# Performance work log

Hardware: AMD Instinct MI355X
Metric: run time of the kernel (lower is better)

## Reference

```python
import jax, jax.numpy as jnp
import numpy as np

N = 100000          # num nodes
E = 1600000         # num edges (before self loops)
IN_C = 128
OUT_C = 64
RATIO = 0.5
NEG_SLOPE = 0.2


def setup_inputs() -> dict:
    key = jax.random.key(0)
    k1, k2, k3, k4, k5 = jax.random.split(key, 5)
    x = jax.random.normal(k1, (N, IN_C), jnp.float32)
    # edges with no self loops (module removes then re-adds self loops)
    src = jax.random.randint(k2, (E,), 0, N, dtype=jnp.int32)
    off = jax.random.randint(k3, (E,), 1, N, dtype=jnp.int32)
    tgt = (src + off) % N
    edge_index = jnp.stack([src, tgt])  # [2, E], row0=source(j), row1=target(i)
    # glorot init
    s_w = float(np.sqrt(6.0 / (IN_C + OUT_C)))
    weight = jax.random.uniform(k4, (IN_C, OUT_C), jnp.float32, -s_w, s_w)
    s_a = float(np.sqrt(6.0 / (1 + 2 * OUT_C)))
    att = jax.random.uniform(k5, (1, 2 * OUT_C), jnp.float32, -s_a, s_a)
    batch = jnp.zeros((N,), jnp.int32)  # single graph
    return {"x": x, "weight": weight, "att": att,
            "edge_index": edge_index, "batch": batch, "bn": 0}


def reference(x, weight, att, edge_index, batch, bn):
    # add self loops (static shapes: E + N edges)
    loops = jnp.arange(N, dtype=edge_index.dtype)
    src = jnp.concatenate([edge_index[0], loops])  # edge_index_j (source)
    tgt = jnp.concatenate([edge_index[1], loops])  # edge_index_i (target)

    h = x @ weight                      # [N, OUT_C]
    x_j = h[src]                        # [E+N, OUT_C] gathered source feats
    x_i = h[tgt]

    # alpha = (cat([x_i, x_j]) * att).sum(-1)
    alpha = x_i @ att[0, :OUT_C] + x_j @ att[0, OUT_C:]   # [E+N]
    alpha = jnp.where(alpha > 0, alpha, NEG_SLOPE * alpha)  # leaky_relu

    # edge-softmax grouped by target node (every node has a self loop -> no empty segment)
    m = jax.ops.segment_max(alpha, tgt, num_segments=N)
    a = jnp.exp(alpha - m[tgt])
    denom = jax.ops.segment_sum(a, tgt, num_segments=N)
    alpha = a / (denom[tgt] + 1e-16)

    # node importance = sum of attention over outgoing edges (grouped by source)
    alpha_sum = jax.ops.segment_sum(alpha, src, num_segments=N)

    # topk node selection (ratio of all nodes; single graph)
    k = int(np.ceil(RATIO * N))
    _, topk_idx = jax.lax.top_k(alpha_sum, k)
    node_mask = jnp.zeros((N,), bool).at[topk_idx].set(True)

    # filter_dn: keep edges whose both endpoints survive; mask instead of compacting
    edge_mask = node_mask[src] & node_mask[tgt]
    alpha_m = jnp.where(edge_mask, alpha, 0.0)

    # weighted scatter-add aggregation to target nodes (aggr='add')
    out = jax.ops.segment_sum(alpha_m[:, None] * x_j, tgt, num_segments=N)  # [N, OUT_C]
    # bn flag is 0 -> BatchNorm skipped
    return out, edge_mask, node_mask
```

## Files before the change

### kernel.cpp

```cpp
#include <hip/hip_runtime.h>
#include <stdint.h>

#define IN_C 128
#define OUT_C 64
#define NEG_SLOPE 0.2f
#define RB 256
#define RBINS 512
#define STAGE 8192
#define NGH (RBINS * RB)
#define NGHS (RBINS * RBINS)
#define KC 8
#define SXW 384

typedef unsigned int u32;
typedef unsigned long long u64;

__device__ __forceinline__ u32 fenc(float f) {
  u32 u = __float_as_uint(f);
  return (u & 0x80000000u) ? ~u : (u | 0x80000000u);
}
__device__ __forceinline__ u64 key64(float v, int i) {
  return (((u64)fenc(v)) << 32) | (u64)(0xffffffffu - (u32)i);
}

__global__ __launch_bounds__(256) void k_gemm(const float* __restrict__ x,
                                              const float* __restrict__ w,
                                              const float* __restrict__ att,
                                              float* __restrict__ h,
                                              float* __restrict__ ai, float* __restrict__ aj,
                                              int N) {
  __shared__ float sw[IN_C * OUT_C];
  __shared__ float sx[KC * SXW];
  int tid = threadIdx.x;
  int rbase = blockIdx.x * 256;

  for (int i = tid; i < (IN_C * OUT_C) / 4; i += 256)
    ((float4*)sw)[i] = ((const float4*)w)[i];

  int c0 = (tid & 7) * 8;
  int rg = tid >> 3;
  int sxbase = rg * 12;
  float acc[8][8];
#pragma unroll
  for (int i = 0; i < 8; i++)
#pragma unroll
    for (int j = 0; j < 8; j++) acc[i][j] = 0.f;

  int str = tid >> 1;
  int skq = tid & 1;

  for (int kb = 0; kb < IN_C; kb += KC) {
    __syncthreads();
#pragma unroll
    for (int it = 0; it < 2; ++it) {
      int r = str + it * 128;
      int grow = rbase + r;
      float4 v = make_float4(0.f, 0.f, 0.f, 0.f);
      if (grow < N) v = *(const float4*)&x[(size_t)grow * IN_C + kb + skq * 4];
      int base = (r >> 3) * 12 + (r & 7);
      sx[(skq * 4 + 0) * SXW + base] = v.x;
      sx[(skq * 4 + 1) * SXW + base] = v.y;
      sx[(skq * 4 + 2) * SXW + base] = v.z;
      sx[(skq * 4 + 3) * SXW + base] = v.w;
    }
    __syncthreads();
#pragma unroll
    for (int kl = 0; kl < KC; ++kl) {
      int kg = kb + kl;
      float xr[8], wv[8];
      *(float4*)&xr[0] = *(const float4*)&sx[kl * SXW + sxbase];
      *(float4*)&xr[4] = *(const float4*)&sx[kl * SXW + sxbase + 4];
      *(float4*)&wv[0] = *(const float4*)&sw[kg * OUT_C + c0];
      *(float4*)&wv[4] = *(const float4*)&sw[kg * OUT_C + c0 + 4];
#pragma unroll
      for (int i = 0; i < 8; ++i)
#pragma unroll
        for (int j = 0; j < 8; ++j)
          acc[i][j] += xr[i] * wv[j];
    }
  }

  float pi[8], pj[8];
#pragma unroll
  for (int i = 0; i < 8; ++i) { pi[i] = 0.f; pj[i] = 0.f; }
#pragma unroll
  for (int j = 0; j < 8; ++j) {
    float a0 = att[c0 + j], a1 = att[OUT_C + c0 + j];
#pragma unroll
    for (int i = 0; i < 8; ++i) {
      pi[i] += acc[i][j] * a0;
      pj[i] += acc[i][j] * a1;
    }
  }
#pragma unroll
  for (int o = 1; o < 8; o <<= 1) {
#pragma unroll
    for (int i = 0; i < 8; ++i) {
      pi[i] += __shfl_xor(pi[i], o);
      pj[i] += __shfl_xor(pj[i], o);
    }
  }
#pragma unroll
  for (int i = 0; i < 8; ++i) {
    int row = rbase + rg * 8 + i;
    if (row < N) {
      *(float4*)&h[(size_t)row * OUT_C + c0]     = make_float4(acc[i][0], acc[i][1], acc[i][2], acc[i][3]);
      *(float4*)&h[(size_t)row * OUT_C + c0 + 4] = make_float4(acc[i][4], acc[i][5], acc[i][6], acc[i][7]);
      if ((tid & 7) == 0) { ai[row] = pi[i]; aj[row] = pj[i]; }
    }
  }
}

__global__ __launch_bounds__(256) void k_rhist_t(const int* __restrict__ tgt,
                                                 int E, int EN, int chunk, u32* __restrict__ gh,
                                                 u32* __restrict__ hist8, u32* __restrict__ done,
                                                 u32* __restrict__ sel, u32* __restrict__ cnt, u32 k) {
  __shared__ u32 lh[RBINS];
  int tid = threadIdx.x, b = blockIdx.x;
  if (b == 0) {
    for (int i = tid; i < 2048; i += 256) hist8[i] = 0u;
    if (tid < 8) { done[tid] = 0u; cnt[tid] = 0u; }
    if (tid == 0) { sel[0] = 0u; sel[1] = 0u; sel[2] = k; sel[3] = 0u; }
  }
  for (int d = tid; d < RBINS; d += 256) lh[d] = 0u;
  __syncthreads();
  int lo = b * chunk, hi = min(lo + chunk, EN);
  for (int e = lo + tid; e < hi; e += 256) {
    int t = (e < E) ? tgt[e] : e - E;
    atomicAdd(&lh[((u32)t) >> 8], 1u);
  }
  __syncthreads();
  for (int d = tid; d < RBINS; d += 256) gh[d * RB + b] = lh[d];
}

__global__ __launch_bounds__(256) void k_scanA(const u32* __restrict__ in, u32* __restrict__ out,
                                               u32* __restrict__ bsum, int n) {
  __shared__ u32 s[256];
  int i = blockIdx.x * 256 + threadIdx.x;
  u32 v = (i < n) ? in[i] : 0u;
  s[threadIdx.x] = v;
  __syncthreads();
  for (int o = 1; o < 256; o <<= 1) {
    u32 t = (threadIdx.x >= (unsigned)o) ? s[threadIdx.x - o] : 0u;
    __syncthreads();
    s[threadIdx.x] += t;
    __syncthreads();
  }
  if (i < n) out[i] = s[threadIdx.x] - v;
  if (threadIdx.x == 255) bsum[blockIdx.x] = s[255];
}

__global__ __launch_bounds__(1024) void k_scanB(u32* __restrict__ bsum, int nb) {
  __shared__ u32 s[1024];
  int tid = threadIdx.x;
  u32 v = (tid < nb) ? bsum[tid] : 0u;
  s[tid] = v;
  __syncthreads();
  for (int o = 1; o < 1024; o <<= 1) {
    u32 t = (tid >= o) ? s[tid - o] : 0u;
    __syncthreads();
    s[tid] += t;
    __syncthreads();
  }
  if (tid < nb) bsum[tid] = s[tid] - v;
}

__global__ __launch_bounds__(256) void k_scanC(u32* __restrict__ out, const u32* __restrict__ bsum, int n) {
  int i = blockIdx.x * 256 + threadIdx.x;
  if (i < n) out[i] += bsum[blockIdx.x];
}

__global__ __launch_bounds__(256) void k_rscatter_t(const int* __restrict__ src, const int* __restrict__ tgt,
                                                    int E, int EN, int chunk,
                                                    const u32* __restrict__ gh, u32* __restrict__ bufB) {
  __shared__ u32 cnt[RBINS];
  int tid = threadIdx.x, b = blockIdx.x;
  for (int d = tid; d < RBINS; d += 256) cnt[d] = gh[d * RB + b];
  __syncthreads();
  int lo = b * chunk, hi = min(lo + chunk, EN);
  for (int e = lo + tid; e < hi; e += 256) {
    int s, t;
    if (e < E) { s = src[e]; t = tgt[e]; } else { s = t = e - E; }
    u32 p = atomicAdd(&cnt[((u32)t) >> 8], 1u);
    bufB[p] = (((u32)t & 255u) << 24) | (u32)s;
  }
}

__global__ __launch_bounds__(256) void k_rpass2(const u32* __restrict__ in, u32* __restrict__ out,
                                                const u32* __restrict__ gh, u32* __restrict__ ghs,
                                                u32* __restrict__ offT,
                                                const float* __restrict__ ai, const float* __restrict__ aj,
                                                float* __restrict__ alpha,
                                                int N, int EN) {
  __shared__ u32 hist[256];
  __shared__ u32 sc[256];
  __shared__ u32 lhs[RBINS];
  __shared__ u32 stage[STAGE];
  int tid = threadIdx.x, d = blockIdx.x;
  u32 start = gh[d * RB];
  u32 end = (d < RBINS - 1) ? gh[(d + 1) * RB] : (u32)EN;
  int sz = (int)(end - start);
  hist[tid] = 0u;
  for (int dd = tid; dd < RBINS; dd += 256) lhs[dd] = 0u;
  __syncthreads();
  for (u32 p = start + tid; p < end; p += 256) {
    u32 it = in[p];
    atomicAdd(&hist[it >> 24], 1u);
    atomicAdd(&lhs[(it & 0xffffffu) >> 8], 1u);
  }
  __syncthreads();
  for (int dd = tid; dd < RBINS; dd += 256) ghs[dd * RBINS + d] = lhs[dd];
  u32 hv = hist[tid];
  sc[tid] = hv;
  __syncthreads();
  for (int o = 1; o < 256; o <<= 1) {
    u32 t = (tid >= o) ? sc[tid - o] : 0u;
    __syncthreads();
    sc[tid] += t;
    __syncthreads();
  }
  u32 excl = sc[tid] - hv;
  int node = (d << 8) + tid;
  if (node < N) offT[node] = start + excl;
  if (node == 0) offT[N] = (u32)EN;
  hist[tid] = excl;
  __syncthreads();
  bool staged = (sz <= STAGE);
  for (u32 p = start + tid; p < end; p += 256) {
    u32 it = in[p];
    u32 lp = atomicAdd(&hist[it >> 24], 1u);
    if (staged) stage[lp] = it;
    else out[start + lp] = it;
  }
  __syncthreads();
  if (staged)
    for (int i = tid; i < sz; i += 256) out[start + i] = stage[i];
  __syncthreads();
  if (node < N) {
    int lb = (tid > 0) ? (int)sc[tid - 1] : 0;
    int le = (int)sc[tid];
    float an = ai[node];
    float mx = -1e30f;
    for (int i = lb; i < le; ++i) {
      u32 it = staged ? stage[i] : out[start + i];
      float a = an + aj[it & 0xffffffu];
      a = a > 0.f ? a : NEG_SLOPE * a;
      mx = fmaxf(mx, a);
      if (staged) stage[i] = __float_as_uint(a);
    }
    float sm = 0.f;
    for (int i = lb; i < le; ++i) {
      float a;
      if (staged) a = __uint_as_float(stage[i]);
      else {
        u32 it = out[start + i];
        a = an + aj[it & 0xffffffu];
        a = a > 0.f ? a : NEG_SLOPE * a;
      }
      float v = expf(a - mx);
      sm += v;
      if (staged) stage[i] = __float_as_uint(v);
      else alpha[start + i] = v;
    }
    float inv = 1.f / (sm + 1e-16f);
    for (int i = lb; i < le; ++i) {
      float v = staged ? __uint_as_float(stage[i]) : alpha[start + i];
      alpha[start + i] = v * inv;
    }
  }
}

__global__ __launch_bounds__(256) void k_rscatter_s(const u32* __restrict__ csr,
                                                    const float* __restrict__ alpha,
                                                    const u32* __restrict__ gh, const u32* __restrict__ ghs,
                                                    u64* __restrict__ bufB, int EN) {
  __shared__ u32 cnt[RBINS];
  int tid = threadIdx.x, d = blockIdx.x;
  for (int dd = tid; dd < RBINS; dd += 256) cnt[dd] = ghs[dd * RBINS + d];
  __syncthreads();
  u32 start = gh[d * RB];
  u32 end = (d < RBINS - 1) ? gh[(d + 1) * RB] : (u32)EN;
  for (u32 e = start + tid; e < end; e += 256) {
    u32 s = csr[e] & 0xffffffu;
    u32 p = atomicAdd(&cnt[s >> 8], 1u);
    bufB[p] = (((u64)(s & 255u)) << 32) | __float_as_uint(alpha[e]);
  }
}

__global__ __launch_bounds__(256) void k_asum_acc(const u64* __restrict__ bufB,
                                                  const u32* __restrict__ ghs,
                                                  float* __restrict__ asum, int N, int EN) {
  __shared__ float sums[256];
  int tid = threadIdx.x, d = blockIdx.x;
  u32 start = ghs[d * RBINS];
  u32 end = (d < RBINS - 1) ? ghs[(d + 1) * RBINS] : (u32)EN;
  sums[tid] = 0.f;
  __syncthreads();
  for (u32 p = start + tid; p < end; p += 256) {
    u64 it = bufB[p];
    atomicAdd(&sums[(u32)(it >> 32)], __uint_as_float((u32)it));
  }
  __syncthreads();
  int node = d * 256 + tid;
  if (node < N) asum[node] = sums[tid];
}

__global__ __launch_bounds__(256) void k_histpick(const float* __restrict__ asum,
                                                  const u32* __restrict__ list_in, const u32* __restrict__ cnt_in,
                                                  u32* __restrict__ list_out, u32* __restrict__ cnt_out,
                                                  u32* __restrict__ hist8, u32* __restrict__ done,
                                                  u32* __restrict__ sel, int N, int pass, int nblk) {
  __shared__ u32 lh[256];
  __shared__ u32 sres;
  __shared__ u32 s[256];
  int tid = threadIdx.x;
  lh[tid] = 0u;
  __syncthreads();
  u64 prefix = ((const u64*)sel)[0];
  int shift = 56 - 8 * pass;
  int n = list_in ? (int)*cnt_in : N;
  int i = blockIdx.x * 256 + tid;
  if (i < n) {
    int idx = list_in ? (int)list_in[i] : i;
    u64 k = key64(asum[idx], idx);
    bool ok = (pass == 0) || ((k >> (shift + 8)) == prefix);
    if (ok) {
      atomicAdd(&lh[(u32)(k >> shift) & 255u], 1u);
      if (list_out) {
        u32 p = atomicAdd(cnt_out, 1u);
        list_out[p] = (u32)idx;
      }
    }
  }
  __syncthreads();
  if (lh[tid]) atomicAdd(&hist8[pass * 256 + tid], lh[tid]);
  __syncthreads();
  if (tid == 0)
    sres = __hip_atomic_fetch_add(&done[pass], 1u, __ATOMIC_ACQ_REL, __HIP_MEMORY_SCOPE_AGENT);
  __syncthreads();
  if (sres == (u32)(nblk - 1)) {
    u32 krem = sel[2];
    u32 hv = __hip_atomic_load(&hist8[pass * 256 + (255 - tid)], __ATOMIC_RELAXED,
                               __HIP_MEMORY_SCOPE_AGENT);
    s[tid] = hv;
    __syncthreads();
    for (int o = 1; o < 256; o <<= 1) {
      u32 t = (tid >= o) ? s[tid - o] : 0u;
      __syncthreads();
      s[tid] += t;
      __syncthreads();
    }
    u32 cum = s[tid], prev = (tid > 0) ? s[tid - 1] : 0u;
    if (cum >= krem && prev < krem) {
      int dsel = 255 - tid;
      ((u64*)sel)[0] = (prefix << 8) | (u64)(u32)dsel;
      sel[2] = krem - prev;
    }
  }
}

__global__ __launch_bounds__(256) void k_finish(const float* __restrict__ asum,
                                                const u32* __restrict__ list, const u32* __restrict__ cntp,
                                                u32* __restrict__ sel) {
  __shared__ u64 keys[2048];
  __shared__ u32 cc;
  int tid = threadIdx.x;
  if (tid == 0) cc = 0u;
  __syncthreads();
  int n = (int)*cntp;
  u32 fsel = (u32)((const u64*)sel)[0];
  u32 krem = sel[2];
  for (int i = tid; i < n; i += 256) {
    int idx = (int)list[i];
    u64 k = key64(asum[idx], idx);
    if ((u32)(k >> 32) == fsel) {
      u32 p = atomicAdd(&cc, 1u);
      if (p < 2048) keys[p] = k;
    }
  }
  __syncthreads();
  int C = (int)min(cc, 2048u);
  for (int i = tid; i < C; i += 256) {
    u64 k = keys[i];
    u32 rank = 0;
    for (int j = 0; j < C; ++j)
      if (keys[j] > k) rank++;
    if (rank == krem - 1) ((u64*)sel)[0] = k;
  }
}

__global__ __launch_bounds__(256) void k_node_mask(const float* __restrict__ asum,
                                                   const u32* __restrict__ sel,
                                                   u32* __restrict__ nm,
                                                   float* __restrict__ out_node, int N) {
  int i = blockIdx.x * 256 + threadIdx.x;
  if (i >= N) return;
  u64 T = ((const u64*)sel)[0];
  bool m = key64(asum[i], i) >= T;
  nm[i] = m ? 1u : 0u;
  out_node[i] = m ? 1.f : 0.f;
}

__global__ __launch_bounds__(256) void k_mask(const int* __restrict__ src, const int* __restrict__ tgt,
                                              const u32* __restrict__ nm,
                                              const u32* __restrict__ csr, const float* __restrict__ alpha,
                                              float* __restrict__ out_edge, u64* __restrict__ pair,
                                              int E, int EN) {
  int e = blockIdx.x * 256 + threadIdx.x;
  if (e >= EN) return;
  int s, t;
  if (e < E) { s = src[e]; t = tgt[e]; } else { s = t = e - E; }
  out_edge[e] = (nm[s] && nm[t]) ? 1.f : 0.f;
  u32 sp = csr[e] & 0xffffffu;
  u32 ab = nm[sp] ? __float_as_uint(alpha[e]) : 0u;
  pair[e] = (((u64)sp) << 32) | ab;
}

__global__ __launch_bounds__(256) void k_aggregate(const u32* __restrict__ off,
                                                   const u64* __restrict__ pair,
                                                   const float* __restrict__ h,
                                                   const u32* __restrict__ nm,
                                                   float* __restrict__ out, int N) {
  int node = blockIdx.x * 4 + (threadIdx.x >> 6);
  int lane = threadIdx.x & 63;
  int g = lane >> 4;
  int c = lane & 15;
  if (node >= N) return;
  float4 acc = make_float4(0.f, 0.f, 0.f, 0.f);
  if (nm[node]) {
    u32 b = off[node], e2 = off[node + 1];
    for (u32 p0 = b; p0 < e2; p0 += 16) {
      u64 pr[4];
      float av[4];
      u32 sv[4];
#pragma unroll
      for (int q = 0; q < 4; ++q) {
        u32 p = p0 + q * 4 + (u32)g;
        bool ok = p < e2;
        pr[q] = pair[ok ? p : b];
        av[q] = ok ? __uint_as_float((u32)pr[q]) : 0.f;
        sv[q] = (u32)(pr[q] >> 32);
      }
      float4 hv[4];
#pragma unroll
      for (int q = 0; q < 4; ++q)
        hv[q] = *(const float4*)&h[(size_t)sv[q] * OUT_C + c * 4];
#pragma unroll
      for (int q = 0; q < 4; ++q) {
        acc.x += av[q] * hv[q].x;
        acc.y += av[q] * hv[q].y;
        acc.z += av[q] * hv[q].z;
        acc.w += av[q] * hv[q].w;
      }
    }
#pragma unroll
    for (int o = 16; o < 64; o <<= 1) {
      acc.x += __shfl_xor(acc.x, o);
      acc.y += __shfl_xor(acc.y, o);
      acc.z += __shfl_xor(acc.z, o);
      acc.w += __shfl_xor(acc.w, o);
    }
  }
  if (g == 0)
    *(float4*)&out[(size_t)node * OUT_C + c * 4] = acc;
}

extern "C" void kernel_launch(void* const* d_in, const int* in_sizes, int n_in,
                              void* d_out, int out_size, void* d_ws, size_t ws_size,
                              hipStream_t stream) {
  const float* x   = (const float*)d_in[0];
  const float* w   = (const float*)d_in[1];
  const float* att = (const float*)d_in[2];
  const int*   ei  = (const int*)d_in[3];

  int N = in_sizes[0] / IN_C;
  int E = in_sizes[3] / 2;
  int EN = E + N;
  const int* src = ei;
  const int* tgt = ei + E;

  float* out      = (float*)d_out;
  float* out_edge = out + (size_t)N * OUT_C;
  float* out_node = out_edge + (size_t)EN;

  char* p = (char*)d_ws;
  auto alloc = [&](size_t bytes) -> char* {
    char* r = p;
    p += (bytes + 255) & ~(size_t)255;
    return r;
  };
  float* h     = (float*)alloc((size_t)N * OUT_C * 4);
  float* ai    = (float*)alloc((size_t)N * 4);
  float* aj    = (float*)alloc((size_t)N * 4);
  u32*   bufA  = (u32*)alloc((size_t)EN * 4);
  u64*   bufB  = (u64*)alloc((size_t)EN * 8);
  float* alpha = (float*)alloc((size_t)EN * 4);
  u32*   offT  = (u32*)alloc((size_t)(N + 1) * 4);
  u32*   gh    = (u32*)alloc((size_t)NGH * 4);
  u32*   ghs   = (u32*)alloc((size_t)NGHS * 4);
  u32*   bsum  = (u32*)alloc(2048 * 4);
  float* asum  = (float*)alloc((size_t)N * 4);
  u32*   nm    = (u32*)alloc((size_t)N * 4);
  u32*   hist8 = (u32*)alloc(2048 * 4);
  u32*   done  = (u32*)alloc(8 * 4);
  u32*   cnt   = (u32*)alloc(8 * 4);
  u32*   sel   = (u32*)alloc(256);
  u32*   listA = (u32*)alloc((size_t)N * 4);
  u32*   listB = (u32*)alloc((size_t)N * 4);

  u32 kSel = (u32)((N + 1) / 2);
  int chunk = (EN + RB - 1) / RB;
  int nScanT = (NGH + 255) / 256;
  int nScanS = (NGHS + 255) / 256;
  int gRow = (N + 255) / 256;
  int gN = (N + 255) / 256;
  int gE = (EN + 255) / 256;
  int gNode4 = (N + 3) / 4;

  k_gemm<<<gRow, 256, 0, stream>>>(x, w, att, h, ai, aj, N);

  k_rhist_t<<<RB, 256, 0, stream>>>(tgt, E, EN, chunk, gh, hist8, done, sel, cnt, kSel);
  k_scanA<<<nScanT, 256, 0, stream>>>(gh, gh, bsum, NGH);
  k_scanB<<<1, 1024, 0, stream>>>(bsum, nScanT);
  k_scanC<<<nScanT, 256, 0, stream>>>(gh, bsum, NGH);
  k_rscatter_t<<<RB, 256, 0, stream>>>(src, tgt, E, EN, chunk, gh, (u32*)bufB);
  k_rpass2<<<RBINS, 256, 0, stream>>>((u32*)bufB, bufA, gh, ghs, offT, ai, aj, alpha, N, EN);

  k_scanA<<<nScanS, 256, 0, stream>>>(ghs, ghs, bsum, NGHS);
  k_scanB<<<1, 1024, 0, stream>>>(bsum, nScanS);
  k_scanC<<<nScanS, 256, 0, stream>>>(ghs, bsum, NGHS);
  k_rscatter_s<<<RBINS, 256, 0, stream>>>(bufA, alpha, gh, ghs, bufB, EN);
  k_asum_acc<<<RBINS, 256, 0, stream>>>(bufB, ghs, asum, N, EN);

  k_histpick<<<gN, 256, 0, stream>>>(asum, nullptr, nullptr, nullptr, nullptr,
                                     hist8, done, sel, N, 0, gN);
  k_histpick<<<gN, 256, 0, stream>>>(asum, nullptr, nullptr, listA, &cnt[1],
                                     hist8, done, sel, N, 1, gN);
  k_histpick<<<gN, 256, 0, stream>>>(asum, listA, &cnt[1], listB, &cnt[2],
                                     hist8, done, sel, N, 2, gN);
  k_histpick<<<gN, 256, 0, stream>>>(asum, listB, &cnt[2], listA, &cnt[3],
                                     hist8, done, sel, N, 3, gN);
  k_finish<<<1, 256, 0, stream>>>(asum, listA, &cnt[3], sel);

  k_node_mask<<<gN, 256, 0, stream>>>(asum, sel, nm, out_node, N);
  k_mask<<<gE, 256, 0, stream>>>(src, tgt, nm, bufA, alpha, out_edge, bufB, E, EN);
  k_aggregate<<<gNode4, 256, 0, stream>>>(offT, bufB, h, nm, out, N);
}
```

Before: 372.9 us.

## Single-pass decoupled-lookback scan, retiled GEMM, half-wave aggregation

Replaces the three-kernel scan (block scan, block-sum scan, add-back) with a single-pass decoupled-lookback scan that uses ticket-ordered blocks and per-block state flags. This removes four launches and the extra passes over the histogram arrays. The GEMM is retiled to 128-thread blocks of 128 rows with KC=16 and coalesced row loads into shared memory, and aggregation now uses 32 lanes per node with 8 gathers in flight. The lookback spin-waits and the smaller GEMM blocks, which reload the weight matrix more often, add serialisation and extra traffic in exchange.

```diff
diff --git a/kernel.cpp b/kernel.cpp
--- a/kernel.cpp
+++ b/kernel.cpp
@@ -9,8 +9,8 @@
 #define STAGE 8192
 #define NGH (RBINS * RB)
 #define NGHS (RBINS * RBINS)
-#define KC 8
-#define SXW 384
+#define KC 16
+#define GROWS 128
 
 typedef unsigned int u32;
 typedef unsigned long long u64;
@@ -23,53 +23,53 @@
   return (((u64)fenc(v)) << 32) | (u64)(0xffffffffu - (u32)i);
 }
 
-__global__ __launch_bounds__(256) void k_gemm(const float* __restrict__ x,
+__global__ __launch_bounds__(128) void k_gemm(const float* __restrict__ x,
                                               const float* __restrict__ w,
                                               const float* __restrict__ att,
                                               float* __restrict__ h,
                                               float* __restrict__ ai, float* __restrict__ aj,
                                               int N) {
   __shared__ float sw[IN_C * OUT_C];
-  __shared__ float sx[KC * SXW];
+  __shared__ float sx[KC * GROWS];
   int tid = threadIdx.x;
-  int rbase = blockIdx.x * 256;
-
-  for (int i = tid; i < (IN_C * OUT_C) / 4; i += 256)
+  int rbase = blockIdx.x * GROWS;
+
+  for (int i = tid; i < (IN_C * OUT_C) / 4; i += 128)
     ((float4*)sw)[i] = ((const float4*)w)[i];
 
-  int c0 = (tid & 7) * 8;
-  int rg = tid >> 3;
-  int sxbase = rg * 12;
+  int cg = tid & 7, rg = tid >> 3;
+  int c0 = cg * 8, r0 = rg * 8;
   float acc[8][8];
 #pragma unroll
   for (int i = 0; i < 8; i++)
 #pragma unroll
     for (int j = 0; j < 8; j++) acc[i][j] = 0.f;
 
-  int str = tid >> 1;
-  int skq = tid & 1;
-
   for (int kb = 0; kb < IN_C; kb += KC) {
     __syncthreads();
-#pragma unroll
-    for (int it = 0; it < 2; ++it) {
-      int r = str + it * 128;
-      int grow = rbase + r;
-      float4 v = make_float4(0.f, 0.f, 0.f, 0.f);
-      if (grow < N) v = *(const float4*)&x[(size_t)grow * IN_C + kb + skq * 4];
-      int base = (r >> 3) * 12 + (r & 7);
-      sx[(skq * 4 + 0) * SXW + base] = v.x;
-      sx[(skq * 4 + 1) * SXW + base] = v.y;
-      sx[(skq * 4 + 2) * SXW + base] = v.z;
-      sx[(skq * 4 + 3) * SXW + base] = v.w;
+    {
+      int grow = rbase + tid;
+      float4 v0 = make_float4(0.f,0.f,0.f,0.f), v1 = v0, v2 = v0, v3 = v0;
+      if (grow < N) {
+        const float4* xp = (const float4*)&x[(size_t)grow * IN_C + kb];
+        v0 = xp[0]; v1 = xp[1]; v2 = xp[2]; v3 = xp[3];
+      }
+      sx[ 0*GROWS + tid] = v0.x; sx[ 1*GROWS + tid] = v0.y;
+      sx[ 2*GROWS + tid] = v0.z; sx[ 3*GROWS + tid] = v0.w;
+      sx[ 4*GROWS + tid] = v1.x; sx[ 5*GROWS + tid] = v1.y;
+      sx[ 6*GROWS + tid] = v1.z; sx[ 7*GROWS + tid] = v1.w;
+      sx[ 8*GROWS + tid] = v2.x; sx[ 9*GROWS + tid] = v2.y;
+      sx[10*GROWS + tid] = v2.z; sx[11*GROWS + tid] = v2.w;
+      sx[12*GROWS + tid] = v3.x; sx[13*GROWS + tid] = v3.y;
+      sx[14*GROWS + tid] = v3.z; sx[15*GROWS + tid] = v3.w;
     }
     __syncthreads();
 #pragma unroll
     for (int kl = 0; kl < KC; ++kl) {
       int kg = kb + kl;
       float xr[8], wv[8];
-      *(float4*)&xr[0] = *(const float4*)&sx[kl * SXW + sxbase];
-      *(float4*)&xr[4] = *(const float4*)&sx[kl * SXW + sxbase + 4];
+      *(float4*)&xr[0] = *(const float4*)&sx[kl * GROWS + r0];
+      *(float4*)&xr[4] = *(const float4*)&sx[kl * GROWS + r0 + 4];
       *(float4*)&wv[0] = *(const float4*)&sw[kg * OUT_C + c0];
       *(float4*)&wv[4] = *(const float4*)&sw[kg * OUT_C + c0 + 4];
 #pragma unroll
@@ -102,11 +102,11 @@
   }
 #pragma unroll
   for (int i = 0; i < 8; ++i) {
-    int row = rbase + rg * 8 + i;
+    int row = rbase + r0 + i;
     if (row < N) {
       *(float4*)&h[(size_t)row * OUT_C + c0]     = make_float4(acc[i][0], acc[i][1], acc[i][2], acc[i][3]);
       *(float4*)&h[(size_t)row * OUT_C + c0 + 4] = make_float4(acc[i][4], acc[i][5], acc[i][6], acc[i][7]);
-      if ((tid & 7) == 0) { ai[row] = pi[i]; aj[row] = pj[i]; }
+      if (cg == 0) { ai[row] = pi[i]; aj[row] = pj[i]; }
     }
   }
 }
@@ -114,12 +114,17 @@
 __global__ __launch_bounds__(256) void k_rhist_t(const int* __restrict__ tgt,
                                                  int E, int EN, int chunk, u32* __restrict__ gh,
                                                  u32* __restrict__ hist8, u32* __restrict__ done,
-                                                 u32* __restrict__ sel, u32* __restrict__ cnt, u32 k) {
+                                                 u32* __restrict__ sel, u32* __restrict__ cnt, u32 k,
+                                                 u64* __restrict__ stateT, u64* __restrict__ stateS,
+                                                 u32* __restrict__ tickets) {
   __shared__ u32 lh[RBINS];
   int tid = threadIdx.x, b = blockIdx.x;
   if (b == 0) {
     for (int i = tid; i < 2048; i += 256) hist8[i] = 0u;
+    for (int i = tid; i < 512;  i += 256) stateT[i] = 0ull;
+    for (int i = tid; i < 1024; i += 256) stateS[i] = 0ull;
     if (tid < 8) { done[tid] = 0u; cnt[tid] = 0u; }
+    if (tid < 2) tickets[tid] = 0u;
     if (tid == 0) { sel[0] = 0u; sel[1] = 0u; sel[2] = k; sel[3] = 0u; }
   }
   for (int d = tid; d < RBINS; d += 256) lh[d] = 0u;
@@ -133,41 +138,47 @@
   for (int d = tid; d < RBINS; d += 256) gh[d * RB + b] = lh[d];
 }
 
-__global__ __launch_bounds__(256) void k_scanA(const u32* __restrict__ in, u32* __restrict__ out,
-                                               u32* __restrict__ bsum, int n) {
+__global__ __launch_bounds__(256) void k_scan(u32* __restrict__ data, int n,
+                                              u32* __restrict__ ticket, u64* __restrict__ state) {
   __shared__ u32 s[256];
-  int i = blockIdx.x * 256 + threadIdx.x;
-  u32 v = (i < n) ? in[i] : 0u;
-  s[threadIdx.x] = v;
+  __shared__ u32 sticket;
+  __shared__ u32 sprefix;
+  int tid = threadIdx.x;
+  if (tid == 0)
+    sticket = __hip_atomic_fetch_add(ticket, 1u, __ATOMIC_RELAXED, __HIP_MEMORY_SCOPE_AGENT);
+  __syncthreads();
+  u32 b = sticket;
+  int i = (int)b * 256 + tid;
+  u32 v = (i < n) ? data[i] : 0u;
+  s[tid] = v;
   __syncthreads();
   for (int o = 1; o < 256; o <<= 1) {
-    u32 t = (threadIdx.x >= (unsigned)o) ? s[threadIdx.x - o] : 0u;
-    __syncthreads();
-    s[threadIdx.x] += t;
-    __syncthreads();
-  }
-  if (i < n) out[i] = s[threadIdx.x] - v;
-  if (threadIdx.x == 255) bsum[blockIdx.x] = s[255];
-}
-
-__global__ __launch_bounds__(1024) void k_scanB(u32* __restrict__ bsum, int nb) {
-  __shared__ u32 s[1024];
-  int tid = threadIdx.x;
-  u32 v = (tid < nb) ? bsum[tid] : 0u;
-  s[tid] = v;
-  __syncthreads();
-  for (int o = 1; o < 1024; o <<= 1) {
     u32 t = (tid >= o) ? s[tid - o] : 0u;
     __syncthreads();
     s[tid] += t;
     __syncthreads();
   }
-  if (tid < nb) bsum[tid] = s[tid] - v;
-}
-
-__global__ __launch_bounds__(256) void k_scanC(u32* __restrict__ out, const u32* __restrict__ bsum, int n) {
-  int i = blockIdx.x * 256 + threadIdx.x;
-  if (i < n) out[i] += bsum[blockIdx.x];
+  if (tid == 0) {
+    u32 total = s[255];
+    __hip_atomic_store(&state[b], (1ull << 32) | (u64)total, __ATOMIC_RELEASE,
+                       __HIP_MEMORY_SCOPE_AGENT);
+    u32 pref = 0;
+    int j = (int)b - 1;
+    while (j >= 0) {
+      u64 st;
+      do {
+        st = __hip_atomic_load(&state[j], __ATOMIC_ACQUIRE, __HIP_MEMORY_SCOPE_AGENT);
+      } while ((st >> 32) == 0ull);
+      pref += (u32)st;
+      if ((st >> 32) == 2ull) break;
+      --j;
+    }
+    __hip_atomic_store(&state[b], (2ull << 32) | (u64)(pref + total), __ATOMIC_RELEASE,
+                       __HIP_MEMORY_SCOPE_AGENT);
+    sprefix = pref;
+  }
+  __syncthreads();
+  if (i < n) data[i] = sprefix + s[tid] - v;
 }
 
 __global__ __launch_bounds__(256) void k_rscatter_t(const int* __restrict__ src, const int* __restrict__ tgt,
@@ -421,45 +432,42 @@
                                                    const float* __restrict__ h,
                                                    const u32* __restrict__ nm,
                                                    float* __restrict__ out, int N) {
-  int node = blockIdx.x * 4 + (threadIdx.x >> 6);
-  int lane = threadIdx.x & 63;
-  int g = lane >> 4;
-  int c = lane & 15;
+  int node = blockIdx.x * 8 + (threadIdx.x >> 5);
+  int sub = threadIdx.x & 31;
+  int g = sub >> 4;
+  int c = sub & 15;
   if (node >= N) return;
   float4 acc = make_float4(0.f, 0.f, 0.f, 0.f);
   if (nm[node]) {
     u32 b = off[node], e2 = off[node + 1];
     for (u32 p0 = b; p0 < e2; p0 += 16) {
-      u64 pr[4];
-      float av[4];
-      u32 sv[4];
-#pragma unroll
-      for (int q = 0; q < 4; ++q) {
-        u32 p = p0 + q * 4 + (u32)g;
+      u64 pr[8];
+      float av[8];
+      u32 sv[8];
+#pragma unroll
+      for (int q = 0; q < 8; ++q) {
+        u32 p = p0 + q * 2 + (u32)g;
         bool ok = p < e2;
         pr[q] = pair[ok ? p : b];
         av[q] = ok ? __uint_as_float((u32)pr[q]) : 0.f;
         sv[q] = (u32)(pr[q] >> 32);
       }
-      float4 hv[4];
-#pragma unroll
-      for (int q = 0; q < 4; ++q)
+      float4 hv[8];
+#pragma unroll
+      for (int q = 0; q < 8; ++q)
         hv[q] = *(const float4*)&h[(size_t)sv[q] * OUT_C + c * 4];
 #pragma unroll
-      for (int q = 0; q < 4; ++q) {
+      for (int q = 0; q < 8; ++q) {
         acc.x += av[q] * hv[q].x;
         acc.y += av[q] * hv[q].y;
         acc.z += av[q] * hv[q].z;
         acc.w += av[q] * hv[q].w;
       }
     }
-#pragma unroll
-    for (int o = 16; o < 64; o <<= 1) {
-      acc.x += __shfl_xor(acc.x, o);
-      acc.y += __shfl_xor(acc.y, o);
-      acc.z += __shfl_xor(acc.z, o);
-      acc.w += __shfl_xor(acc.w, o);
-    }
+    acc.x += __shfl_xor(acc.x, 16);
+    acc.y += __shfl_xor(acc.y, 16);
+    acc.z += __shfl_xor(acc.z, 16);
+    acc.w += __shfl_xor(acc.w, 16);
   }
   if (g == 0)
     *(float4*)&out[(size_t)node * OUT_C + c * 4] = acc;
@@ -489,46 +497,43 @@
     p += (bytes + 255) & ~(size_t)255;
     return r;
   };
-  float* h     = (float*)alloc((size_t)N * OUT_C * 4);
-  float* ai    = (float*)alloc((size_t)N * 4);
-  float* aj    = (float*)alloc((size_t)N * 4);
-  u32*   bufA  = (u32*)alloc((size_t)EN * 4);
-  u64*   bufB  = (u64*)alloc((size_t)EN * 8);
-  float* alpha = (float*)alloc((size_t)EN * 4);
-  u32*   offT  = (u32*)alloc((size_t)(N + 1) * 4);
-  u32*   gh    = (u32*)alloc((size_t)NGH * 4);
-  u32*   ghs   = (u32*)alloc((size_t)NGHS * 4);
-  u32*   bsum  = (u32*)alloc(2048 * 4);
-  float* asum  = (float*)alloc((size_t)N * 4);
-  u32*   nm    = (u32*)alloc((size_t)N * 4);
-  u32*   hist8 = (u32*)alloc(2048 * 4);
-  u32*   done  = (u32*)alloc(8 * 4);
-  u32*   cnt   = (u32*)alloc(8 * 4);
-  u32*   sel   = (u32*)alloc(256);
-  u32*   listA = (u32*)alloc((size_t)N * 4);
-  u32*   listB = (u32*)alloc((size_t)N * 4);
+  float* h      = (float*)alloc((size_t)N * OUT_C * 4);
+  float* ai     = (float*)alloc((size_t)N * 4);
+  float* aj     = (float*)alloc((size_t)N * 4);
+  u32*   bufA   = (u32*)alloc((size_t)EN * 4);
+  u64*   bufB   = (u64*)alloc((size_t)EN * 8);
+  float* alpha  = (float*)alloc((size_t)EN * 4);
+  u32*   offT   = (u32*)alloc((size_t)(N + 1) * 4);
+  u32*   gh     = (u32*)alloc((size_t)NGH * 4);
+  u32*   ghs    = (u32*)alloc((size_t)NGHS * 4);
+  float* asum   = (float*)alloc((size_t)N * 4);
+  u32*   nm     = (u32*)alloc((size_t)N * 4);
+  u32*   hist8  = (u32*)alloc(2048 * 4);
+  u32*   done   = (u32*)alloc(8 * 4);
+  u32*   cnt    = (u32*)alloc(8 * 4);
+  u32*   sel    = (u32*)alloc(256);
+  u64*   stateT = (u64*)alloc(512 * 8);
+  u64*   stateS = (u64*)alloc(1024 * 8);
+  u32*   tickets= (u32*)alloc(256);
+  u32*   listA  = (u32*)alloc((size_t)N * 4);
+  u32*   listB  = (u32*)alloc((size_t)N * 4);
 
   u32 kSel = (u32)((N + 1) / 2);
   int chunk = (EN + RB - 1) / RB;
-  int nScanT = (NGH + 255) / 256;
-  int nScanS = (NGHS + 255) / 256;
-  int gRow = (N + 255) / 256;
+  int gRow = (N + GROWS - 1) / GROWS;
   int gN = (N + 255) / 256;
   int gE = (EN + 255) / 256;
-  int gNode4 = (N + 3) / 4;
-
-  k_gemm<<<gRow, 256, 0, stream>>>(x, w, att, h, ai, aj, N);
-
-  k_rhist_t<<<RB, 256, 0, stream>>>(tgt, E, EN, chunk, gh, hist8, done, sel, cnt, kSel);
-  k_scanA<<<nScanT, 256, 0, stream>>>(gh, gh, bsum, NGH);
-  k_scanB<<<1, 1024, 0, stream>>>(bsum, nScanT);
-  k_scanC<<<nScanT, 256, 0, stream>>>(gh, bsum, NGH);
+  int gNode8 = (N + 7) / 8;
+
+  k_gemm<<<gRow, 128, 0, stream>>>(x, w, att, h, ai, aj, N);
+
+  k_rhist_t<<<RB, 256, 0, stream>>>(tgt, E, EN, chunk, gh, hist8, done, sel, cnt, kSel,
+                                    stateT, stateS, tickets);
+  k_scan<<<(NGH + 255) / 256, 256, 0, stream>>>(gh, NGH, &tickets[0], stateT);
   k_rscatter_t<<<RB, 256, 0, stream>>>(src, tgt, E, EN, chunk, gh, (u32*)bufB);
   k_rpass2<<<RBINS, 256, 0, stream>>>((u32*)bufB, bufA, gh, ghs, offT, ai, aj, alpha, N, EN);
 
-  k_scanA<<<nScanS, 256, 0, stream>>>(ghs, ghs, bsum, NGHS);
-  k_scanB<<<1, 1024, 0, stream>>>(bsum, nScanS);
-  k_scanC<<<nScanS, 256, 0, stream>>>(ghs, bsum, NGHS);
+  k_scan<<<(NGHS + 255) / 256, 256, 0, stream>>>(ghs, NGHS, &tickets[1], stateS);
   k_rscatter_s<<<RBINS, 256, 0, stream>>>(bufA, alpha, gh, ghs, bufB, EN);
   k_asum_acc<<<RBINS, 256, 0, stream>>>(bufB, ghs, asum, N, EN);
 
@@ -544,5 +549,5 @@
 
   k_node_mask<<<gN, 256, 0, stream>>>(asum, sel, nm, out_node, N);
   k_mask<<<gE, 256, 0, stream>>>(src, tgt, nm, bufA, alpha, out_edge, bufB, E, EN);
-  k_aggregate<<<gNode4, 256, 0, stream>>>(offT, bufB, h, nm, out, N);
-}
+  k_aggregate<<<gNode8, 256, 0, stream>>>(offT, bufB, h, nm, out, N);
+}
```

Result: slower. 808.8 us (+116.9%).
